# Kernel tuning notes

Measured on AMD Instinct MI355X. Metric: run time of the kernel, lower is better.

The kernel has to match this reference:

```python
import jax, jax.numpy as jnp
import numpy as np

N_NODES = 100000
N_EDGES = 1600000
D_FEAT = 64
H1 = 16
H2 = 1


def setup_inputs() -> dict:
    key = jax.random.key(0)
    ks = jax.random.split(key, 8)
    x = jax.random.normal(ks[0], (N_NODES, D_FEAT), dtype=jnp.float32)
    edge_index = jax.random.randint(ks[1], (2, N_EDGES), 0, N_NODES, dtype=jnp.int64)
    s1 = 1.0 / np.sqrt(D_FEAT)
    s2 = 1.0 / np.sqrt(H1)
    Wl1 = jax.random.uniform(ks[2], (H1, D_FEAT), jnp.float32, -s1, s1)
    Wr1 = jax.random.uniform(ks[3], (H1, D_FEAT), jnp.float32, -s1, s1)
    b1 = jax.random.uniform(ks[4], (H1,), jnp.float32, -s1, s1)
    Wl2 = jax.random.uniform(ks[5], (H2, H1), jnp.float32, -s2, s2)
    Wr2 = jax.random.uniform(ks[6], (H2, H1), jnp.float32, -s2, s2)
    b2 = jax.random.uniform(ks[7], (H2,), jnp.float32, -s2, s2)
    return {"x": x, "edge_index": edge_index, "Wl1": Wl1, "Wr1": Wr1, "b1": b1,
            "Wl2": Wl2, "Wr2": Wr2, "b2": b2}


def _sage_conv(h, src, dst, Wl, Wr, b, n_nodes):
    # mean aggregation of source-node features onto destination nodes
    msg_sum = jax.ops.segment_sum(h[src], dst, num_segments=n_nodes)  # [N, d]
    cnt = jax.ops.segment_sum(jnp.ones((src.shape[0],), h.dtype), dst,
                              num_segments=n_nodes)  # [N]
    mean = msg_sum / jnp.maximum(cnt, 1.0)[:, None]
    # out = lin_l(mean_neighbors) + lin_r(self) + bias
    return mean @ Wl.T + h @ Wr.T + b


def reference(x, edge_index, Wl1, Wr1, b1, Wl2, Wr2, b2):
    src, dst = edge_index[0], edge_index[1]
    n = x.shape[0]
    h = jax.nn.relu(_sage_conv(x, src, dst, Wl1, Wr1, b1, n))
    # F.dropout(training=False) is identity at inference
    out = _sage_conv(h, src, dst, Wl2, Wr2, b2, n)
    return out
```

## Files before the change

kernel.cpp:

```cpp
#include <hip/hip_runtime.h>
#include <hip/hip_fp16.h>

#define H1F 16
#define BSH 9
#define BNODES 512
#define MAXBUCK 256
#define CAPSH 14
#define CAPB (1 << CAPSH)
#define TILE 4096
#define MAXPT 20

union SharedU {
    struct {
        int lhist[MAXBUCK];
        int lbase[MAXBUCK];
        int gbase[MAXBUCK];
        int wsum[8];
        unsigned int stage[TILE];
        unsigned short sbuck[TILE];
    } p;
    struct {
        float4 wl4[16][17];
        float4 wr4[16][17];
    } q;
};

__global__ __launch_bounds__(512) void fused_kernel(
    const float* __restrict__ x,
    const float* __restrict__ Wl1,
    const float* __restrict__ Wr1,
    const float* __restrict__ b1,
    __half* __restrict__ xl,
    float* __restrict__ xr,
    const int* __restrict__ ei,
    int* __restrict__ gcur16,
    unsigned int* __restrict__ edge2,
    int N, int E, int nPart) {
    __shared__ SharedU sh;
    int t = threadIdx.x;

    if ((int)blockIdx.x < nPart) {
        if (t < MAXBUCK) sh.p.lhist[t] = 0;
        __syncthreads();

        int e0 = blockIdx.x * TILE;
        int eb = e0 + t * 8;

        int ss[8], dd[8];
        if (eb + 8 <= E) {
            int4 s0 = *(const int4*)(ei + eb);
            int4 s1 = *(const int4*)(ei + eb + 4);
            int4 d0 = *(const int4*)(ei + E + eb);
            int4 d1 = *(const int4*)(ei + E + eb + 4);
            ss[0]=s0.x; ss[1]=s0.y; ss[2]=s0.z; ss[3]=s0.w;
            ss[4]=s1.x; ss[5]=s1.y; ss[6]=s1.z; ss[7]=s1.w;
            dd[0]=d0.x; dd[1]=d0.y; dd[2]=d0.z; dd[3]=d0.w;
            dd[4]=d1.x; dd[5]=d1.y; dd[6]=d1.z; dd[7]=d1.w;
        } else {
#pragma unroll
            for (int k = 0; k < 8; ++k) {
                int e = eb + k;
                ss[k] = (e < E) ? ei[e] : -1;
                dd[k] = (e < E) ? ei[E + e] : 0;
            }
        }

        unsigned int pk[8];
        int rk[8], bk[8];
#pragma unroll
        for (int k = 0; k < 8; ++k) {
            if (ss[k] >= 0) {
                int b = dd[k] >> BSH;
                bk[k] = b;
                pk[k] = ((unsigned int)ss[k] << BSH) |
                        (unsigned int)(dd[k] & (BNODES - 1));
                rk[k] = atomicAdd(&sh.p.lhist[b], 1);
            } else {
                bk[k] = -1;
            }
        }
        __syncthreads();

        int cnt = E - e0; if (cnt > TILE) cnt = TILE;

        int v = 0, s = 0;
        int lane = t & 63, wid = t >> 6;
        if (t < MAXBUCK) {
            v = sh.p.lhist[t];
            if (v > 0)
                sh.p.gbase[t] = (t << CAPSH) + atomicAdd(&gcur16[t * 16], v);
            s = v;
#pragma unroll
            for (int d = 1; d < 64; d <<= 1) {
                int u = __shfl_up(s, d);
                if (lane >= d) s += u;
            }
            if (lane == 63) sh.p.wsum[wid] = s;
        }
        __syncthreads();
        if (t < MAXBUCK) {
            int wofs = 0;
            for (int w = 0; w < wid; ++w) wofs += sh.p.wsum[w];
            sh.p.lbase[t] = wofs + s - v;
        }
        __syncthreads();

#pragma unroll
        for (int k = 0; k < 8; ++k) {
            if (bk[k] >= 0) {
                int p = sh.p.lbase[bk[k]] + rk[k];
                sh.p.stage[p] = pk[k];
                sh.p.sbuck[p] = (unsigned short)bk[k];
            }
        }
        __syncthreads();

        for (int i = t; i < cnt; i += 512) {
            int b = sh.p.sbuck[i];
            int idx = sh.p.gbase[b] + (i - sh.p.lbase[b]);
            if (idx < ((b + 1) << CAPSH)) edge2[idx] = sh.p.stage[i];
        }
    } else {
        if (t < 256) {
            ((float4*)&sh.q.wl4[t >> 4][t & 15])[0] = ((const float4*)Wl1)[t];
        } else {
            int u = t - 256;
            ((float4*)&sh.q.wr4[u >> 4][u & 15])[0] = ((const float4*)Wr1)[u];
        }
        __syncthreads();

        int f = t & 15;
        int nl = t >> 4;
        float bf = b1[f];
        int blk = blockIdx.x - nPart;
        const float4* x4 = (const float4*)x;

#pragma unroll
        for (int rep = 0; rep < 4; ++rep) {
            int gn = blk * 128 + rep * 32 + nl;
            if (gn < N) {
                float al = 0.0f, ar = 0.0f;
#pragma unroll
                for (int k4 = 0; k4 < 16; ++k4) {
                    float4 xv = x4[(size_t)gn * 16 + k4];
                    float4 a = sh.q.wl4[f][k4];
                    float4 b = sh.q.wr4[f][k4];
                    al += xv.x * a.x + xv.y * a.y + xv.z * a.z + xv.w * a.w;
                    ar += xv.x * b.x + xv.y * b.y + xv.z * b.z + xv.w * b.w;
                }
                xl[(size_t)gn * H1F + f] = __float2half(al);
                xr[(size_t)gn * H1F + f] = ar + bf;
            }
        }
    }
}

__global__ __launch_bounds__(512) void sort2_kernel(
    const unsigned int* __restrict__ edge2,
    const int* __restrict__ gcur16,
    int* __restrict__ csr,
    int* __restrict__ offp,
    int* __restrict__ degv,
    int N) {
    __shared__ int h[BNODES];
    __shared__ int wsum[8];

    int t = threadIdx.x;
    int b = blockIdx.x;
    int n0 = b << BSH;
    int e0 = b << CAPSH;
    int cnt = gcur16[b * 16];
    if (cnt > MAXPT * 512) cnt = MAXPT * 512;

    h[t] = 0;
    __syncthreads();

    unsigned int rw[MAXPT];
#pragma unroll
    for (int k = 0; k < MAXPT; ++k) {
        int idx = k * 512 + t;
        rw[k] = (idx < cnt) ? edge2[e0 + idx] : 0xFFFFFFFFu;
    }

#pragma unroll
    for (int k = 0; k < MAXPT; ++k)
        if (rw[k] != 0xFFFFFFFFu) atomicAdd(&h[rw[k] & (BNODES - 1)], 1);
    __syncthreads();

    int v = h[t];
    int lane = t & 63, wid = t >> 6;
    int s = v;
#pragma unroll
    for (int d = 1; d < 64; d <<= 1) {
        int u = __shfl_up(s, d);
        if (lane >= d) s += u;
    }
    if (lane == 63) wsum[wid] = s;
    __syncthreads();
    int wofs = 0;
    for (int w = 0; w < wid; ++w) wofs += wsum[w];
    int excl = wofs + s - v;

    int gn = n0 + t;
    if (gn < N) {
        degv[gn] = v;
        offp[gn] = e0 + excl;
    }
    __syncthreads();
    h[t] = excl;
    __syncthreads();

#pragma unroll
    for (int k = 0; k < MAXPT; ++k) {
        if (rw[k] != 0xFFFFFFFFu) {
            int d = (int)(rw[k] & (BNODES - 1));
            int pos = atomicAdd(&h[d], 1);
            csr[e0 + pos] = (int)(rw[k] >> BSH);
        }
    }
}

__global__ void gather1_kernel(const int* __restrict__ csr,
                               const int* __restrict__ offp,
                               const int* __restrict__ degv,
                               const __half2* __restrict__ xl2,
                               const float2* __restrict__ xr2,
                               const float* __restrict__ Wl2,
                               const float* __restrict__ Wr2,
                               const float* __restrict__ b2,
                               float* __restrict__ hl2,
                               float* __restrict__ outp,
                               int N, int nbuck) {
    int g = blockIdx.x;
    int xcd = g & 7, r = g >> 3;
    int bi = r >> 4, k = r & 15;
    int b = bi * 8 + xcd;
    if (b >= nbuck) return;
    int node = (b << BSH) + (k << 5) + (threadIdx.x >> 3);
    int l = threadIdx.x & 7;
    if (node >= N) return;

    int d = degv[node];
    const int* row = csr + offp[node];

    float sx = 0.0f, sy = 0.0f;
    int j = 0;
    for (; j + 4 <= d; j += 4) {
        int s0 = row[j], s1 = row[j + 1], s2 = row[j + 2], s3 = row[j + 3];
        float2 v0 = __half22float2(xl2[(size_t)s0 * 8 + l]);
        float2 v1 = __half22float2(xl2[(size_t)s1 * 8 + l]);
        float2 v2 = __half22float2(xl2[(size_t)s2 * 8 + l]);
        float2 v3 = __half22float2(xl2[(size_t)s3 * 8 + l]);
        sx += v0.x + v1.x + v2.x + v3.x;
        sy += v0.y + v1.y + v2.y + v3.y;
    }
    for (; j < d; ++j) {
        float2 v = __half22float2(xl2[(size_t)row[j] * 8 + l]);
        sx += v.x; sy += v.y;
    }

    float inv = 1.0f / fmaxf((float)d, 1.0f);
    float2 xrv = xr2[(size_t)node * 8 + l];
    float h0 = fmaxf(sx * inv + xrv.x, 0.0f);
    float h1 = fmaxf(sy * inv + xrv.y, 0.0f);
    float2 wlv = ((const float2*)Wl2)[l];
    float2 wrv = ((const float2*)Wr2)[l];
    float pl = h0 * wlv.x + h1 * wlv.y;
    float pr = h0 * wrv.x + h1 * wrv.y;
#pragma unroll
    for (int off = 4; off; off >>= 1) {
        pl += __shfl_xor(pl, off);
        pr += __shfl_xor(pr, off);
    }
    if (l == 0) {
        hl2[node] = pl;
        outp[node] = pr + b2[0];
    }
}

__global__ void gather2_kernel(const int* __restrict__ csr,
                               const int* __restrict__ offp,
                               const int* __restrict__ degv,
                               const float* __restrict__ hl2,
                               const float* __restrict__ outp,
                               float* __restrict__ out,
                               int N, int nbuck) {
    int g = blockIdx.x;
    int xcd = g & 7, r = g >> 3;
    int bi = r >> 3, k = r & 7;
    int b = bi * 8 + xcd;
    if (b >= nbuck) return;
    int node = (b << BSH) + (k << 6) + (threadIdx.x >> 2);
    int l = threadIdx.x & 3;
    if (node >= N) return;

    int d = degv[node];
    const int* row = csr + offp[node];

    float s = 0.0f;
    for (int j = l; j < d; j += 4) s += hl2[row[j]];
    s += __shfl_xor(s, 1);
    s += __shfl_xor(s, 2);
    if (l == 0) out[node] = s / fmaxf((float)d, 1.0f) + outp[node];
}

extern "C" void kernel_launch(void* const* d_in, const int* in_sizes, int n_in,
                              void* d_out, int out_size, void* d_ws, size_t ws_size,
                              hipStream_t stream) {
    const float* x   = (const float*)d_in[0];
    const int*   ei  = (const int*)d_in[1];
    const float* Wl1 = (const float*)d_in[2];
    const float* Wr1 = (const float*)d_in[3];
    const float* b1  = (const float*)d_in[4];
    const float* Wl2 = (const float*)d_in[5];
    const float* Wr2 = (const float*)d_in[6];
    const float* b2  = (const float*)d_in[7];
    float* out = (float*)d_out;

    int N = in_sizes[0] / 64;
    int E = in_sizes[1] / 2;
    int nbuck = (N + BNODES - 1) >> BSH;

    size_t win = (size_t)nbuck << CAPSH;
    int* gcur16 = (int*)d_ws;
    unsigned int* edge2 = (unsigned int*)(gcur16 + MAXBUCK * 16);
    int*   csr  = (int*)(edge2 + win);
    int*   offp = csr + win;
    int*   degv = offp + N;
    __half* xl  = (__half*)(degv + N);
    float* xr   = (float*)(xl + (size_t)16 * N);
    float* hl2  = xr + (size_t)16 * N;
    float* outp = hl2 + N;

    int nPart = (E + TILE - 1) / TILE;
    int nProj = (N + 127) / 128;

    (void)hipMemsetAsync(gcur16, 0, MAXBUCK * 16 * sizeof(int), stream);

    fused_kernel<<<nPart + nProj, 512, 0, stream>>>(
        x, Wl1, Wr1, b1, xl, xr, ei, gcur16, edge2, N, E, nPart);

    sort2_kernel<<<nbuck, 512, 0, stream>>>(edge2, gcur16, csr, offp, degv, N);

    int grid1 = 8 * ((nbuck + 7) / 8) * 16;
    gather1_kernel<<<grid1, 256, 0, stream>>>(
        csr, offp, degv, (const __half2*)xl, (const float2*)xr,
        Wl2, Wr2, b2, hl2, outp, N, nbuck);

    int grid2 = 8 * ((nbuck + 7) / 8) * 8;
    gather2_kernel<<<grid2, 256, 0, stream>>>(
        csr, offp, degv, hl2, outp, out, N, nbuck);
}
```

Before: 79.75 us.

## Halve bucket size and fuse projection with per-bucket sort instead of partition

Destination buckets shrink from 512 to 256 nodes, which doubles their count to 391 and gives each bucket a 8192-slot capacity. This gives the bucket sort more blocks to spread across CUs. The node projection now shares a kernel with the per-bucket sort instead of the edge partition, so the partition step runs alone and the sort overlaps with the projection. The gather grids are adjusted to match the new bucket size. The risk is bucket overflow: capacity is 8192 slots while about 4096 edges are expected per bucket, and MAXPT*512 equals the capacity, so no edges are dropped.

```diff
diff --git a/kernel.cpp b/kernel.cpp
--- a/kernel.cpp
+++ b/kernel.cpp
@@ -2,123 +2,185 @@
 #include <hip/hip_fp16.h>
 
 #define H1F 16
-#define BSH 9
-#define BNODES 512
-#define MAXBUCK 256
-#define CAPSH 14
+#define BSH 8
+#define BNODES 256
+#define MAXBUCK 512
+#define CAPSH 13
 #define CAPB (1 << CAPSH)
 #define TILE 4096
-#define MAXPT 20
+#define MAXPT 16
+
+__global__ __launch_bounds__(512) void part_kernel(
+    const int* __restrict__ ei,
+    int* __restrict__ gcur16,
+    unsigned int* __restrict__ edge2,
+    int E) {
+    __shared__ int lhist[MAXBUCK];
+    __shared__ int lbase[MAXBUCK];
+    __shared__ int gbase[MAXBUCK];
+    __shared__ int wsum[8];
+    __shared__ unsigned int stage[TILE];
+    __shared__ unsigned short sbuck[TILE];
+
+    int t = threadIdx.x;
+    lhist[t] = 0;
+    __syncthreads();
+
+    int e0 = blockIdx.x * TILE;
+    int eb = e0 + t * 8;
+
+    int ss[8], dd[8];
+    if (eb + 8 <= E) {
+        int4 s0 = *(const int4*)(ei + eb);
+        int4 s1 = *(const int4*)(ei + eb + 4);
+        int4 d0 = *(const int4*)(ei + E + eb);
+        int4 d1 = *(const int4*)(ei + E + eb + 4);
+        ss[0]=s0.x; ss[1]=s0.y; ss[2]=s0.z; ss[3]=s0.w;
+        ss[4]=s1.x; ss[5]=s1.y; ss[6]=s1.z; ss[7]=s1.w;
+        dd[0]=d0.x; dd[1]=d0.y; dd[2]=d0.z; dd[3]=d0.w;
+        dd[4]=d1.x; dd[5]=d1.y; dd[6]=d1.z; dd[7]=d1.w;
+    } else {
+#pragma unroll
+        for (int k = 0; k < 8; ++k) {
+            int e = eb + k;
+            ss[k] = (e < E) ? ei[e] : -1;
+            dd[k] = (e < E) ? ei[E + e] : 0;
+        }
+    }
+
+    unsigned int pk[8];
+    int rk[8], bk[8];
+#pragma unroll
+    for (int k = 0; k < 8; ++k) {
+        if (ss[k] >= 0) {
+            int b = dd[k] >> BSH;
+            bk[k] = b;
+            pk[k] = ((unsigned int)ss[k] << BSH) |
+                    (unsigned int)(dd[k] & (BNODES - 1));
+            rk[k] = atomicAdd(&lhist[b], 1);
+        } else {
+            bk[k] = -1;
+        }
+    }
+    __syncthreads();
+
+    int cnt = E - e0; if (cnt > TILE) cnt = TILE;
+
+    int v = lhist[t];
+    if (v > 0) gbase[t] = (t << CAPSH) + atomicAdd(&gcur16[t * 16], v);
+    int lane = t & 63, wid = t >> 6;
+    int s = v;
+#pragma unroll
+    for (int d = 1; d < 64; d <<= 1) {
+        int u = __shfl_up(s, d);
+        if (lane >= d) s += u;
+    }
+    if (lane == 63) wsum[wid] = s;
+    __syncthreads();
+    int wofs = 0;
+    for (int w = 0; w < wid; ++w) wofs += wsum[w];
+    lbase[t] = wofs + s - v;
+    __syncthreads();
+
+#pragma unroll
+    for (int k = 0; k < 8; ++k) {
+        if (bk[k] >= 0) {
+            int p = lbase[bk[k]] + rk[k];
+            stage[p] = pk[k];
+            sbuck[p] = (unsigned short)bk[k];
+        }
+    }
+    __syncthreads();
+
+    for (int i = t; i < cnt; i += 512) {
+        int b = sbuck[i];
+        int idx = gbase[b] + (i - lbase[b]);
+        if (idx < ((b + 1) << CAPSH)) edge2[idx] = stage[i];
+    }
+}
 
 union SharedU {
     struct {
-        int lhist[MAXBUCK];
-        int lbase[MAXBUCK];
-        int gbase[MAXBUCK];
-        int wsum[8];
-        unsigned int stage[TILE];
-        unsigned short sbuck[TILE];
-    } p;
+        int h[BNODES];
+        int wsum[4];
+    } s;
     struct {
         float4 wl4[16][17];
         float4 wr4[16][17];
     } q;
 };
 
-__global__ __launch_bounds__(512) void fused_kernel(
+__global__ __launch_bounds__(512) void sortproj_kernel(
+    const unsigned int* __restrict__ edge2,
+    const int* __restrict__ gcur16,
+    int* __restrict__ csr,
+    int* __restrict__ offp,
+    int* __restrict__ degv,
     const float* __restrict__ x,
     const float* __restrict__ Wl1,
     const float* __restrict__ Wr1,
     const float* __restrict__ b1,
     __half* __restrict__ xl,
     float* __restrict__ xr,
-    const int* __restrict__ ei,
-    int* __restrict__ gcur16,
-    unsigned int* __restrict__ edge2,
-    int N, int E, int nPart) {
+    int N, int nSort) {
     __shared__ SharedU sh;
     int t = threadIdx.x;
 
-    if ((int)blockIdx.x < nPart) {
-        if (t < MAXBUCK) sh.p.lhist[t] = 0;
-        __syncthreads();
-
-        int e0 = blockIdx.x * TILE;
-        int eb = e0 + t * 8;
-
-        int ss[8], dd[8];
-        if (eb + 8 <= E) {
-            int4 s0 = *(const int4*)(ei + eb);
-            int4 s1 = *(const int4*)(ei + eb + 4);
-            int4 d0 = *(const int4*)(ei + E + eb);
-            int4 d1 = *(const int4*)(ei + E + eb + 4);
-            ss[0]=s0.x; ss[1]=s0.y; ss[2]=s0.z; ss[3]=s0.w;
-            ss[4]=s1.x; ss[5]=s1.y; ss[6]=s1.z; ss[7]=s1.w;
-            dd[0]=d0.x; dd[1]=d0.y; dd[2]=d0.z; dd[3]=d0.w;
-            dd[4]=d1.x; dd[5]=d1.y; dd[6]=d1.z; dd[7]=d1.w;
-        } else {
-#pragma unroll
-            for (int k = 0; k < 8; ++k) {
-                int e = eb + k;
-                ss[k] = (e < E) ? ei[e] : -1;
-                dd[k] = (e < E) ? ei[E + e] : 0;
-            }
-        }
-
-        unsigned int pk[8];
-        int rk[8], bk[8];
-#pragma unroll
-        for (int k = 0; k < 8; ++k) {
-            if (ss[k] >= 0) {
-                int b = dd[k] >> BSH;
-                bk[k] = b;
-                pk[k] = ((unsigned int)ss[k] << BSH) |
-                        (unsigned int)(dd[k] & (BNODES - 1));
-                rk[k] = atomicAdd(&sh.p.lhist[b], 1);
-            } else {
-                bk[k] = -1;
-            }
-        }
-        __syncthreads();
-
-        int cnt = E - e0; if (cnt > TILE) cnt = TILE;
-
+    if ((int)blockIdx.x < nSort) {
+        int b = blockIdx.x;
+        int n0 = b << BSH;
+        int e0 = b << CAPSH;
+        int cnt = gcur16[b * 16];
+        if (cnt > CAPB) cnt = CAPB;
+
+        if (t < BNODES) sh.s.h[t] = 0;
+        __syncthreads();
+
+        unsigned int rw[MAXPT];
+#pragma unroll
+        for (int k = 0; k < MAXPT; ++k) {
+            int idx = k * 512 + t;
+            rw[k] = (idx < cnt) ? edge2[e0 + idx] : 0xFFFFFFFFu;
+        }
+
+#pragma unroll
+        for (int k = 0; k < MAXPT; ++k)
+            if (rw[k] != 0xFFFFFFFFu) atomicAdd(&sh.s.h[rw[k] & (BNODES - 1)], 1);
+        __syncthreads();
+
+        int lane = t & 63, wid = t >> 6;
         int v = 0, s = 0;
-        int lane = t & 63, wid = t >> 6;
-        if (t < MAXBUCK) {
-            v = sh.p.lhist[t];
-            if (v > 0)
-                sh.p.gbase[t] = (t << CAPSH) + atomicAdd(&gcur16[t * 16], v);
+        if (t < BNODES) {
+            v = sh.s.h[t];
             s = v;
 #pragma unroll
             for (int d = 1; d < 64; d <<= 1) {
                 int u = __shfl_up(s, d);
                 if (lane >= d) s += u;
             }
-            if (lane == 63) sh.p.wsum[wid] = s;
-        }
-        __syncthreads();
-        if (t < MAXBUCK) {
+            if (lane == 63) sh.s.wsum[wid] = s;
+        }
+        __syncthreads();
+        if (t < BNODES) {
             int wofs = 0;
-            for (int w = 0; w < wid; ++w) wofs += sh.p.wsum[w];
-            sh.p.lbase[t] = wofs + s - v;
-        }
-        __syncthreads();
-
-#pragma unroll
-        for (int k = 0; k < 8; ++k) {
-            if (bk[k] >= 0) {
-                int p = sh.p.lbase[bk[k]] + rk[k];
-                sh.p.stage[p] = pk[k];
-                sh.p.sbuck[p] = (unsigned short)bk[k];
+            for (int w = 0; w < wid; ++w) wofs += sh.s.wsum[w];
+            int excl = wofs + s - v;
+            int gn = n0 + t;
+            if (gn < N) {
+                degv[gn] = v;
+                offp[gn] = e0 + excl;
             }
-        }
-        __syncthreads();
-
-        for (int i = t; i < cnt; i += 512) {
-            int b = sh.p.sbuck[i];
-            int idx = sh.p.gbase[b] + (i - sh.p.lbase[b]);
-            if (idx < ((b + 1) << CAPSH)) edge2[idx] = sh.p.stage[i];
+            sh.s.h[t] = excl;
+        }
+        __syncthreads();
+
+#pragma unroll
+        for (int k = 0; k < MAXPT; ++k) {
+            if (rw[k] != 0xFFFFFFFFu) {
+                int d = (int)(rw[k] & (BNODES - 1));
+                int pos = atomicAdd(&sh.s.h[d], 1);
+                csr[e0 + pos] = (int)(rw[k] >> BSH);
+            }
         }
     } else {
         if (t < 256) {
@@ -132,7 +194,7 @@
         int f = t & 15;
         int nl = t >> 4;
         float bf = b1[f];
-        int blk = blockIdx.x - nPart;
+        int blk = blockIdx.x - nSort;
         const float4* x4 = (const float4*)x;
 
 #pragma unroll
@@ -151,71 +213,6 @@
                 xl[(size_t)gn * H1F + f] = __float2half(al);
                 xr[(size_t)gn * H1F + f] = ar + bf;
             }
-        }
-    }
-}
-
-__global__ __launch_bounds__(512) void sort2_kernel(
-    const unsigned int* __restrict__ edge2,
-    const int* __restrict__ gcur16,
-    int* __restrict__ csr,
-    int* __restrict__ offp,
-    int* __restrict__ degv,
-    int N) {
-    __shared__ int h[BNODES];
-    __shared__ int wsum[8];
-
-    int t = threadIdx.x;
-    int b = blockIdx.x;
-    int n0 = b << BSH;
-    int e0 = b << CAPSH;
-    int cnt = gcur16[b * 16];
-    if (cnt > MAXPT * 512) cnt = MAXPT * 512;
-
-    h[t] = 0;
-    __syncthreads();
-
-    unsigned int rw[MAXPT];
-#pragma unroll
-    for (int k = 0; k < MAXPT; ++k) {
-        int idx = k * 512 + t;
-        rw[k] = (idx < cnt) ? edge2[e0 + idx] : 0xFFFFFFFFu;
-    }
-
-#pragma unroll
-    for (int k = 0; k < MAXPT; ++k)
-        if (rw[k] != 0xFFFFFFFFu) atomicAdd(&h[rw[k] & (BNODES - 1)], 1);
-    __syncthreads();
-
-    int v = h[t];
-    int lane = t & 63, wid = t >> 6;
-    int s = v;
-#pragma unroll
-    for (int d = 1; d < 64; d <<= 1) {
-        int u = __shfl_up(s, d);
-        if (lane >= d) s += u;
-    }
-    if (lane == 63) wsum[wid] = s;
-    __syncthreads();
-    int wofs = 0;
-    for (int w = 0; w < wid; ++w) wofs += wsum[w];
-    int excl = wofs + s - v;
-
-    int gn = n0 + t;
-    if (gn < N) {
-        degv[gn] = v;
-        offp[gn] = e0 + excl;
-    }
-    __syncthreads();
-    h[t] = excl;
-    __syncthreads();
-
-#pragma unroll
-    for (int k = 0; k < MAXPT; ++k) {
-        if (rw[k] != 0xFFFFFFFFu) {
-            int d = (int)(rw[k] & (BNODES - 1));
-            int pos = atomicAdd(&h[d], 1);
-            csr[e0 + pos] = (int)(rw[k] >> BSH);
         }
     }
 }
@@ -233,7 +230,7 @@
                                int N, int nbuck) {
     int g = blockIdx.x;
     int xcd = g & 7, r = g >> 3;
-    int bi = r >> 4, k = r & 15;
+    int bi = r >> 3, k = r & 7;
     int b = bi * 8 + xcd;
     if (b >= nbuck) return;
     int node = (b << BSH) + (k << 5) + (threadIdx.x >> 3);
@@ -287,7 +284,7 @@
                                int N, int nbuck) {
     int g = blockIdx.x;
     int xcd = g & 7, r = g >> 3;
-    int bi = r >> 3, k = r & 7;
+    int bi = r >> 2, k = r & 3;
     int b = bi * 8 + xcd;
     if (b >= nbuck) return;
     int node = (b << BSH) + (k << 6) + (threadIdx.x >> 2);
@@ -337,17 +334,18 @@
 
     (void)hipMemsetAsync(gcur16, 0, MAXBUCK * 16 * sizeof(int), stream);
 
-    fused_kernel<<<nPart + nProj, 512, 0, stream>>>(
-        x, Wl1, Wr1, b1, xl, xr, ei, gcur16, edge2, N, E, nPart);
-
-    sort2_kernel<<<nbuck, 512, 0, stream>>>(edge2, gcur16, csr, offp, degv, N);
-
-    int grid1 = 8 * ((nbuck + 7) / 8) * 16;
+    part_kernel<<<nPart, 512, 0, stream>>>(ei, gcur16, edge2, E);
+
+    sortproj_kernel<<<nbuck + nProj, 512, 0, stream>>>(
+        edge2, gcur16, csr, offp, degv,
+        x, Wl1, Wr1, b1, xl, xr, N, nbuck);
+
+    int grid1 = 8 * ((nbuck + 7) / 8) * 8;
     gather1_kernel<<<grid1, 256, 0, stream>>>(
         csr, offp, degv, (const __half2*)xl, (const float2*)xr,
         Wl2, Wr2, b2, hl2, outp, N, nbuck);
 
-    int grid2 = 8 * ((nbuck + 7) / 8) * 8;
+    int grid2 = 8 * ((nbuck + 7) / 8) * 4;
     gather2_kernel<<<grid2, 256, 0, stream>>>(
         csr, offp, degv, hl2, outp, out, N, nbuck);
 }
```

Result: no change. 79.48 us (-0.3%).

## Replace CSR sort and gathers with bucketed shared-memory atomic aggregation

Applied to the files above, without the earlier changes.

Removes the second sort pass that built a CSR, and the two per-node gather kernels. The two SAGE aggregations now work directly on destination-bucketed edges, accumulating into shared memory with atomic adds. Buckets shrink to 256 nodes and get eight per-shard counters to spread global atomic contention, each shard capped at 1024 edges. This saves one kernel launch and the CSR write and read traffic. In exchange it relies on heavy LDS float atomics, makes summation order nondeterministic, and can drop edges if a shard overflows its fixed capacity.

```diff
diff --git a/kernel.cpp b/kernel.cpp
--- a/kernel.cpp
+++ b/kernel.cpp
@@ -2,13 +2,12 @@
 #include <hip/hip_fp16.h>
 
 #define H1F 16
-#define BSH 9
-#define BNODES 512
-#define MAXBUCK 256
-#define CAPSH 14
-#define CAPB (1 << CAPSH)
+#define BSH 8
+#define BNODES 256
+#define MAXBUCK 512
+#define CAPSH 13
+#define SSH 10
 #define TILE 4096
-#define MAXPT 20
 
 union SharedU {
     struct {
@@ -33,14 +32,15 @@
     __half* __restrict__ xl,
     float* __restrict__ xr,
     const int* __restrict__ ei,
-    int* __restrict__ gcur16,
+    int* __restrict__ cur8,
     unsigned int* __restrict__ edge2,
     int N, int E, int nPart) {
     __shared__ SharedU sh;
     int t = threadIdx.x;
 
     if ((int)blockIdx.x < nPart) {
-        if (t < MAXBUCK) sh.p.lhist[t] = 0;
+        int shard = blockIdx.x & 7;
+        sh.p.lhist[t] = 0;
         __syncthreads();
 
         int e0 = blockIdx.x * TILE;
@@ -83,26 +83,22 @@
 
         int cnt = E - e0; if (cnt > TILE) cnt = TILE;
 
-        int v = 0, s = 0;
+        int v = sh.p.lhist[t];
+        if (v > 0)
+            sh.p.gbase[t] = (t << CAPSH) + (shard << SSH) +
+                            atomicAdd(&cur8[shard * MAXBUCK + t], v);
         int lane = t & 63, wid = t >> 6;
-        if (t < MAXBUCK) {
-            v = sh.p.lhist[t];
-            if (v > 0)
-                sh.p.gbase[t] = (t << CAPSH) + atomicAdd(&gcur16[t * 16], v);
-            s = v;
-#pragma unroll
-            for (int d = 1; d < 64; d <<= 1) {
-                int u = __shfl_up(s, d);
-                if (lane >= d) s += u;
-            }
-            if (lane == 63) sh.p.wsum[wid] = s;
-        }
-        __syncthreads();
-        if (t < MAXBUCK) {
-            int wofs = 0;
-            for (int w = 0; w < wid; ++w) wofs += sh.p.wsum[w];
-            sh.p.lbase[t] = wofs + s - v;
-        }
+        int s = v;
+#pragma unroll
+        for (int d = 1; d < 64; d <<= 1) {
+            int u = __shfl_up(s, d);
+            if (lane >= d) s += u;
+        }
+        if (lane == 63) sh.p.wsum[wid] = s;
+        __syncthreads();
+        int wofs = 0;
+        for (int w = 0; w < wid; ++w) wofs += sh.p.wsum[w];
+        sh.p.lbase[t] = wofs + s - v;
         __syncthreads();
 
 #pragma unroll
@@ -118,7 +114,8 @@
         for (int i = t; i < cnt; i += 512) {
             int b = sh.p.sbuck[i];
             int idx = sh.p.gbase[b] + (i - sh.p.lbase[b]);
-            if (idx < ((b + 1) << CAPSH)) edge2[idx] = sh.p.stage[i];
+            int shardEnd = (b << CAPSH) + (((blockIdx.x & 7) + 1) << SSH);
+            if (idx < shardEnd) edge2[idx] = sh.p.stage[i];
         }
     } else {
         if (t < 256) {
@@ -155,153 +152,115 @@
     }
 }
 
-__global__ __launch_bounds__(512) void sort2_kernel(
+__global__ __launch_bounds__(512) void aggr1_kernel(
     const unsigned int* __restrict__ edge2,
-    const int* __restrict__ gcur16,
-    int* __restrict__ csr,
-    int* __restrict__ offp,
+    const int* __restrict__ cur8,
+    const __half* __restrict__ xl,
+    const float* __restrict__ xr,
+    const float* __restrict__ Wl2,
+    const float* __restrict__ Wr2,
+    const float* __restrict__ b2,
+    float* __restrict__ hl2,
+    float* __restrict__ outp,
     int* __restrict__ degv,
     int N) {
+    __shared__ float acc[BNODES][17];
     __shared__ int h[BNODES];
-    __shared__ int wsum[8];
 
     int t = threadIdx.x;
     int b = blockIdx.x;
     int n0 = b << BSH;
     int e0 = b << CAPSH;
-    int cnt = gcur16[b * 16];
-    if (cnt > MAXPT * 512) cnt = MAXPT * 512;
-
-    h[t] = 0;
+
+    for (int i = t; i < BNODES * 17; i += 512) ((float*)acc)[i] = 0.0f;
+    if (t < BNODES) h[t] = 0;
     __syncthreads();
 
-    unsigned int rw[MAXPT];
-#pragma unroll
-    for (int k = 0; k < MAXPT; ++k) {
-        int idx = k * 512 + t;
-        rw[k] = (idx < cnt) ? edge2[e0 + idx] : 0xFFFFFFFFu;
-    }
-
-#pragma unroll
-    for (int k = 0; k < MAXPT; ++k)
-        if (rw[k] != 0xFFFFFFFFu) atomicAdd(&h[rw[k] & (BNODES - 1)], 1);
+#pragma unroll
+    for (int s = 0; s < 8; ++s) {
+        int cs = cur8[s * MAXBUCK + b];
+        if (cs > (1 << SSH)) cs = (1 << SSH);
+        int base = e0 + (s << SSH);
+#pragma unroll
+        for (int k = 0; k < 2; ++k) {
+            int idx = (k << 9) + t;
+            if (idx < cs) {
+                unsigned int u = edge2[base + idx];
+                int src = (int)(u >> BSH);
+                int d = (int)(u & (BNODES - 1));
+                const uint4* rp = (const uint4*)(xl + (size_t)src * H1F);
+                uint4 A = rp[0], B = rp[1];
+                unsigned int dw[8] = {A.x, A.y, A.z, A.w, B.x, B.y, B.z, B.w};
+#pragma unroll
+                for (int q = 0; q < 8; ++q) {
+                    __half2 hh = __builtin_bit_cast(__half2, dw[q]);
+                    float2 f2 = __half22float2(hh);
+                    atomicAdd(&acc[d][2 * q], f2.x);
+                    atomicAdd(&acc[d][2 * q + 1], f2.y);
+                }
+                atomicAdd(&h[d], 1);
+            }
+        }
+    }
     __syncthreads();
 
-    int v = h[t];
-    int lane = t & 63, wid = t >> 6;
-    int s = v;
-#pragma unroll
-    for (int d = 1; d < 64; d <<= 1) {
-        int u = __shfl_up(s, d);
-        if (lane >= d) s += u;
-    }
-    if (lane == 63) wsum[wid] = s;
+    if (t < BNODES) {
+        int gn = n0 + t;
+        if (gn < N) {
+            int dg = h[t];
+            float inv = 1.0f / fmaxf((float)dg, 1.0f);
+            float sl = 0.0f, sr = 0.0f;
+#pragma unroll
+            for (int f = 0; f < H1F; ++f) {
+                float hf = fmaxf(acc[t][f] * inv + xr[(size_t)gn * H1F + f], 0.0f);
+                sl += hf * Wl2[f];
+                sr += hf * Wr2[f];
+            }
+            hl2[gn] = sl;
+            outp[gn] = sr + b2[0];
+            degv[gn] = dg;
+        }
+    }
+}
+
+__global__ __launch_bounds__(512) void aggr2_kernel(
+    const unsigned int* __restrict__ edge2,
+    const int* __restrict__ cur8,
+    const int* __restrict__ degv,
+    const float* __restrict__ hl2,
+    const float* __restrict__ outp,
+    float* __restrict__ out,
+    int N) {
+    __shared__ float acc2[BNODES];
+    int t = threadIdx.x;
+    int b = blockIdx.x;
+    int n0 = b << BSH;
+    int e0 = b << CAPSH;
+
+    if (t < BNODES) acc2[t] = 0.0f;
     __syncthreads();
-    int wofs = 0;
-    for (int w = 0; w < wid; ++w) wofs += wsum[w];
-    int excl = wofs + s - v;
-
-    int gn = n0 + t;
-    if (gn < N) {
-        degv[gn] = v;
-        offp[gn] = e0 + excl;
+
+#pragma unroll
+    for (int s = 0; s < 8; ++s) {
+        int cs = cur8[s * MAXBUCK + b];
+        if (cs > (1 << SSH)) cs = (1 << SSH);
+        int base = e0 + (s << SSH);
+#pragma unroll
+        for (int k = 0; k < 2; ++k) {
+            int idx = (k << 9) + t;
+            if (idx < cs) {
+                unsigned int u = edge2[base + idx];
+                atomicAdd(&acc2[u & (BNODES - 1)], hl2[u >> BSH]);
+            }
+        }
     }
     __syncthreads();
-    h[t] = excl;
-    __syncthreads();
-
-#pragma unroll
-    for (int k = 0; k < MAXPT; ++k) {
-        if (rw[k] != 0xFFFFFFFFu) {
-            int d = (int)(rw[k] & (BNODES - 1));
-            int pos = atomicAdd(&h[d], 1);
-            csr[e0 + pos] = (int)(rw[k] >> BSH);
-        }
-    }
-}
-
-__global__ void gather1_kernel(const int* __restrict__ csr,
-                               const int* __restrict__ offp,
-                               const int* __restrict__ degv,
-                               const __half2* __restrict__ xl2,
-                               const float2* __restrict__ xr2,
-                               const float* __restrict__ Wl2,
-                               const float* __restrict__ Wr2,
-                               const float* __restrict__ b2,
-                               float* __restrict__ hl2,
-                               float* __restrict__ outp,
-                               int N, int nbuck) {
-    int g = blockIdx.x;
-    int xcd = g & 7, r = g >> 3;
-    int bi = r >> 4, k = r & 15;
-    int b = bi * 8 + xcd;
-    if (b >= nbuck) return;
-    int node = (b << BSH) + (k << 5) + (threadIdx.x >> 3);
-    int l = threadIdx.x & 7;
-    if (node >= N) return;
-
-    int d = degv[node];
-    const int* row = csr + offp[node];
-
-    float sx = 0.0f, sy = 0.0f;
-    int j = 0;
-    for (; j + 4 <= d; j += 4) {
-        int s0 = row[j], s1 = row[j + 1], s2 = row[j + 2], s3 = row[j + 3];
-        float2 v0 = __half22float2(xl2[(size_t)s0 * 8 + l]);
-        float2 v1 = __half22float2(xl2[(size_t)s1 * 8 + l]);
-        float2 v2 = __half22float2(xl2[(size_t)s2 * 8 + l]);
-        float2 v3 = __half22float2(xl2[(size_t)s3 * 8 + l]);
-        sx += v0.x + v1.x + v2.x + v3.x;
-        sy += v0.y + v1.y + v2.y + v3.y;
-    }
-    for (; j < d; ++j) {
-        float2 v = __half22float2(xl2[(size_t)row[j] * 8 + l]);
-        sx += v.x; sy += v.y;
-    }
-
-    float inv = 1.0f / fmaxf((float)d, 1.0f);
-    float2 xrv = xr2[(size_t)node * 8 + l];
-    float h0 = fmaxf(sx * inv + xrv.x, 0.0f);
-    float h1 = fmaxf(sy * inv + xrv.y, 0.0f);
-    float2 wlv = ((const float2*)Wl2)[l];
-    float2 wrv = ((const float2*)Wr2)[l];
-    float pl = h0 * wlv.x + h1 * wlv.y;
-    float pr = h0 * wrv.x + h1 * wrv.y;
-#pragma unroll
-    for (int off = 4; off; off >>= 1) {
-        pl += __shfl_xor(pl, off);
-        pr += __shfl_xor(pr, off);
-    }
-    if (l == 0) {
-        hl2[node] = pl;
-        outp[node] = pr + b2[0];
-    }
-}
-
-__global__ void gather2_kernel(const int* __restrict__ csr,
-                               const int* __restrict__ offp,
-                               const int* __restrict__ degv,
-                               const float* __restrict__ hl2,
-                               const float* __restrict__ outp,
-                               float* __restrict__ out,
-                               int N, int nbuck) {
-    int g = blockIdx.x;
-    int xcd = g & 7, r = g >> 3;
-    int bi = r >> 3, k = r & 7;
-    int b = bi * 8 + xcd;
-    if (b >= nbuck) return;
-    int node = (b << BSH) + (k << 6) + (threadIdx.x >> 2);
-    int l = threadIdx.x & 3;
-    if (node >= N) return;
-
-    int d = degv[node];
-    const int* row = csr + offp[node];
-
-    float s = 0.0f;
-    for (int j = l; j < d; j += 4) s += hl2[row[j]];
-    s += __shfl_xor(s, 1);
-    s += __shfl_xor(s, 2);
-    if (l == 0) out[node] = s / fmaxf((float)d, 1.0f) + outp[node];
+
+    if (t < BNODES) {
+        int gn = n0 + t;
+        if (gn < N)
+            out[gn] = acc2[t] / fmaxf((float)degv[gn], 1.0f) + outp[gn];
+    }
 }
 
 extern "C" void kernel_launch(void* const* d_in, const int* in_sizes, int n_in,
@@ -322,11 +281,9 @@
     int nbuck = (N + BNODES - 1) >> BSH;
 
     size_t win = (size_t)nbuck << CAPSH;
-    int* gcur16 = (int*)d_ws;
-    unsigned int* edge2 = (unsigned int*)(gcur16 + MAXBUCK * 16);
-    int*   csr  = (int*)(edge2 + win);
-    int*   offp = csr + win;
-    int*   degv = offp + N;
+    int* cur8 = (int*)d_ws;
+    unsigned int* edge2 = (unsigned int*)(cur8 + 8 * MAXBUCK);
+    int*   degv = (int*)(edge2 + win);
     __half* xl  = (__half*)(degv + N);
     float* xr   = (float*)(xl + (size_t)16 * N);
     float* hl2  = xr + (size_t)16 * N;
@@ -335,19 +292,14 @@
     int nPart = (E + TILE - 1) / TILE;
     int nProj = (N + 127) / 128;
 
-    (void)hipMemsetAsync(gcur16, 0, MAXBUCK * 16 * sizeof(int), stream);
+    (void)hipMemsetAsync(cur8, 0, 8 * MAXBUCK * sizeof(int), stream);
 
     fused_kernel<<<nPart + nProj, 512, 0, stream>>>(
-        x, Wl1, Wr1, b1, xl, xr, ei, gcur16, edge2, N, E, nPart);
-
-    sort2_kernel<<<nbuck, 512, 0, stream>>>(edge2, gcur16, csr, offp, degv, N);
-
-    int grid1 = 8 * ((nbuck + 7) / 8) * 16;
-    gather1_kernel<<<grid1, 256, 0, stream>>>(
-        csr, offp, degv, (const __half2*)xl, (const float2*)xr,
-        Wl2, Wr2, b2, hl2, outp, N, nbuck);
-
-    int grid2 = 8 * ((nbuck + 7) / 8) * 8;
-    gather2_kernel<<<grid2, 256, 0, stream>>>(
-        csr, offp, degv, hl2, outp, out, N, nbuck);
+        x, Wl1, Wr1, b1, xl, xr, ei, cur8, edge2, N, E, nPart);
+
+    aggr1_kernel<<<nbuck, 512, 0, stream>>>(
+        edge2, cur8, xl, xr, Wl2, Wr2, b2, hl2, outp, degv, N);
+
+    aggr2_kernel<<<nbuck, 512, 0, stream>>>(
+        edge2, cur8, degv, hl2, outp, out, N);
 }
```

Result: slower. 222.2 us (+178.7%).
